# Kernel tuning notes

Measured on AMD Instinct MI355X. Metric: run time of the kernel, lower is better.

## Reference

```python
import jax, jax.numpy as jnp
import numpy as np

N_NODES = 100000


def _gcn_norm(edge_index, n):
    # PyG GCNConv default: add self-loops, symmetric normalization
    src, dst = edge_index[0], edge_index[1]
    loops = jnp.arange(n, dtype=src.dtype)
    src = jnp.concatenate([src, loops])
    dst = jnp.concatenate([dst, loops])
    deg = jax.ops.segment_sum(jnp.ones_like(dst, dtype=jnp.float32), dst, num_segments=n)
    dinv = jnp.where(deg > 0, jax.lax.rsqrt(deg), 0.0)
    norm = dinv[src] * dinv[dst]  # [E+N]
    return src, dst, norm


def _gcn_conv(x, src, dst, norm, W, b, n):
    h = x @ W                                  # [N, out] transform first
    msg = h[src] * norm[:, None]               # gather + edge weight
    out = jax.ops.segment_sum(msg, dst, num_segments=n)  # scatter-add
    return out + b


def setup_inputs() -> dict:
    key = jax.random.key(0)
    k1, k2, k3, k4 = jax.random.split(key, 4)
    in_f, h_f, out_f = 128, 256, 128
    x = jax.random.normal(k1, (N_NODES, in_f), dtype=jnp.float32)
    edge_index = jax.random.randint(k2, (2, 1600000), 0, N_NODES, dtype=jnp.int64)
    W1 = jax.random.normal(k3, (in_f, h_f), dtype=jnp.float32) / np.sqrt(in_f)
    b1 = jnp.zeros((h_f,), dtype=jnp.float32)
    W2 = jax.random.normal(k4, (h_f, out_f), dtype=jnp.float32) / np.sqrt(h_f)
    b2 = jnp.zeros((out_f,), dtype=jnp.float32)
    return {"x": x, "edge_index": edge_index, "W1": W1, "b1": b1, "W2": W2, "b2": b2}


def reference(x, edge_index, W1, b1, W2, b2):
    n = x.shape[0]
    src, dst, norm = _gcn_norm(edge_index, n)
    h = jax.nn.relu(_gcn_conv(x, src, dst, norm, W1, b1, n))
    return _gcn_conv(h, src, dst, norm, W2, b2, n)
```

## Files before the change

kernel.cpp:

```cpp
#include <hip/hip_runtime.h>

typedef __bf16 bf16x8 __attribute__((ext_vector_type(8)));
typedef float f32x4 __attribute__((ext_vector_type(4)));

#define DEVI static __device__ __forceinline__
#define SCH 8192
#define CAP 49152

DEVI unsigned short f2bf(float f){
  unsigned int x = __builtin_bit_cast(unsigned int, f);
  x = (x + 0x7fffu + ((x >> 16) & 1u)) >> 16;
  return (unsigned short)x;
}
DEVI unsigned int packbf2(float a, float b){
  return (unsigned int)f2bf(a) | ((unsigned int)f2bf(b) << 16);
}
DEVI float bflo(unsigned int u){ return __builtin_bit_cast(float, u << 16); }
DEVI float bfhi(unsigned int u){ return __builtin_bit_cast(float, u & 0xffff0000u); }

__global__ void k_zero(int* __restrict__ p, int n){
  int i = blockIdx.x*256 + threadIdx.x;
  if (i < n) p[i] = 0;
}


__global__ __launch_bounds__(512) void kb_scat1h(const int* __restrict__ src,
    const int* __restrict__ dst, int* __restrict__ cntf, int* __restrict__ cntc,
    int* __restrict__ p1, int E, int NB, int NBC){
  __shared__ int hf[2048];
  __shared__ int baseSh[64];
  __shared__ int hc[64];
  int t = threadIdx.x;
  for (int i=t;i<NB;i+=512) hf[i]=0;
  __syncthreads();
  int base = blockIdx.x*SCH;
  int lim = base+SCH < E ? base+SCH : E;
  for (int i = base+t; i < lim; i += 512)
    atomicAdd(&hf[dst[i]>>8], 1);
  __syncthreads();
  if (t < NBC){
    int s2 = 0;
    int f0 = t*8;
    for (int j=0;j<8;j++){ int f=f0+j; if (f<NB) s2 += hf[f]; }
    baseSh[t] = s2 ? atomicAdd(&cntc[t], s2) : 0;
    hc[t] = 0;
  }
  for (int i=t;i<NB;i+=512)
    if (hf[i]) atomicAdd(&cntf[i], hf[i]);
  __syncthreads();
  for (int i = base+t; i < lim; i += 512){
    int d = dst[i];
    int b = d>>11;
    int r = atomicAdd(&hc[b], 1);
    p1[(size_t)b*CAP + baseSh[b] + r] = (src[i]<<11) | (d & 2047);
  }
}

__global__ __launch_bounds__(256) void kb_scan(const int* __restrict__ cntf,
    int* __restrict__ bucketOff, int* __restrict__ bucketCur, int NB){
  __shared__ int sh[256];
  int t = threadIdx.x;
  int per = (NB+255)/256;
  int vals[8];
  int lsum = 0;
  for (int j=0;j<per;j++){
    int i = t*per+j;
    int v = (i<NB) ? cntf[i] : 0;
    vals[j]=v; lsum+=v;
  }
  sh[t]=lsum; __syncthreads();
  for (int off=1; off<256; off<<=1){
    int x = (t>=off) ? sh[t-off] : 0;
    __syncthreads();
    sh[t] += x;
    __syncthreads();
  }
  int run = sh[t]-lsum;
  for (int j=0;j<per;j++){
    int i = t*per+j;
    if (i<NB){ bucketOff[i]=run; bucketCur[i]=run; }
    run += vals[j];
  }
  if (t==255) bucketOff[NB]=run;
}

__global__ __launch_bounds__(512) void kb_scat2(const int* __restrict__ p1,
    const int* __restrict__ cntc, int* __restrict__ cur,
    int* __restrict__ pk, int NB){
  __shared__ int h[8];
  __shared__ int baseSh[8];
  int t = threadIdx.x;
  int bc = blockIdx.x >> 3;
  int sub = blockIdx.x & 7;
  int s = bc*CAP;
  int e = s + cntc[bc];
  if (t < 8) h[t] = 0;
  __syncthreads();
  for (int i = s + sub*512 + t; i < e; i += 4096)
    atomicAdd(&h[(p1[i]>>8)&7], 1);
  __syncthreads();
  if (t < 8){
    int c2 = h[t];
    baseSh[t] = c2 ? atomicAdd(&cur[bc*8+t], c2) : 0;
    h[t] = 0;
  }
  __syncthreads();
  for (int i = s + sub*512 + t; i < e; i += 4096){
    int p = p1[i];
    int f = (p>>8)&7;
    int r = atomicAdd(&h[f], 1);
    int pos = baseSh[f] + r;
    pk[pos] = ((p>>11)<<8) | (p&255);
  }
}

DEVI void packW(const float* __restrict__ W, unsigned short* __restrict__ Wp,
                int idx, int N, int NF){
  int l = idx & 63;
  int frag = idx >> 6;
  int cf = frag % NF;
  int ks = frag / NF;
  int kbase = ks*32 + (l>>4)*8;
  int col = cf*16 + (l&15);
  unsigned short* dp = Wp + (size_t)idx*8;
  #pragma unroll
  for (int j=0;j<8;j++) dp[j] = f2bf(W[(size_t)(kbase+j)*N + col]);
}

__global__ __launch_bounds__(256) void kb_fused(const int* __restrict__ pk,
    const int* __restrict__ bOff,
    int* __restrict__ rp, int* __restrict__ csr, float* __restrict__ dinv,
    const float2* __restrict__ x2, unsigned int* __restrict__ xb,
    const float* __restrict__ W1, unsigned short* __restrict__ W1p,
    const float* __restrict__ W2, unsigned short* __restrict__ W2p,
    int n, int NB, int E){
  int t = threadIdx.x;
  int b = blockIdx.x;
  if (b >= NB){
    int idx = (b-NB)*256 + t;
    if (idx < 4096) packW(W1, W1p, idx, 256, 16);
    else            packW(W2, W2p, idx-4096, 128, 8);
    return;
  }
  __shared__ int c[256];
  __shared__ int sh[256];
  __shared__ int cur[256];
  __shared__ float dv[256];
  int s = bOff[b], e2 = bOff[b+1];
  c[t]=0; __syncthreads();
  for (int i=s+t;i<e2;i+=256) atomicAdd(&c[pk[i]&255], 1);
  __syncthreads();
  int deg = c[t];
  sh[t]=deg; __syncthreads();
  for (int o=1;o<256;o<<=1){
    int x = (t>=o) ? sh[t-o] : 0;
    __syncthreads();
    sh[t]+=x;
    __syncthreads();
  }
  int excl = sh[t]-deg;
  int node = b*256+t;
  float dnv = rsqrtf((float)(deg+1));
  if (node<n){
    rp[node] = s + excl;
    dinv[node] = dnv;
  }
  if (b==NB-1 && t==0) rp[n] = E;
  cur[t] = s + excl;
  dv[t] = dnv;
  __syncthreads();
  for (int i=s+t;i<e2;i+=256){
    int p = pk[i];
    int r = atomicAdd(&cur[p&255], 1);
    csr[r] = p & (int)0xFFFFFF00u;
  }
  int base_node = b*256;
  int rows = n - base_node; if (rows > 256) rows = 256;
  int j = t & 63;
  for (int rb = t>>6; rb < rows; rb += 4){
    int nd = base_node + rb;
    float d = dv[rb];
    float2 v = x2[(size_t)nd*64 + j];
    xb[(size_t)nd*64 + j] = packbf2(d*v.x, d*v.y);
  }
}

#define ACC8(V) { a0+=bflo(V.x); a1+=bfhi(V.x); a2+=bflo(V.y); a3+=bfhi(V.y); \
                  a4+=bflo(V.z); a5+=bfhi(V.z); a6+=bflo(V.w); a7+=bfhi(V.w); }

template<bool FINAL>
__global__ __launch_bounds__(256) void k_agg(
    const unsigned int* __restrict__ xs, const int* __restrict__ rp,
    const int* __restrict__ csr, const float* __restrict__ dinv,
    const float* __restrict__ bias, unsigned int* __restrict__ outb,
    float* __restrict__ outf, int n){
  int node = blockIdx.x*4 + (threadIdx.x>>6);
  if (node >= n) return;
  int l = threadIdx.x & 63;
  int q = l & 15;
  int h = l >> 4;
  const char* xbase = (const char*)xs;
  float a0=0,a1=0,a2=0,a3=0,a4=0,a5=0,a6=0,a7=0;
  int e = rp[node], end = rp[node+1];
  int p = e;
  int nf = (end - e) >> 4;
  for (int blk=0; blk<nf; ++blk, p+=16){
    uint4 v[4];
    #pragma unroll
    for (int i=0;i<4;i++){
      int boff = csr[p + 4*i + h];
      v[i] = *(const uint4*)(xbase + (size_t)(unsigned)boff + q*16);
    }
    ACC8(v[0]); ACC8(v[1]); ACC8(v[2]); ACC8(v[3]);
  }
  int rem = end - p;
  if (rem >= 8){
    uint4 v[2];
    #pragma unroll
    for (int i=0;i<2;i++){
      int boff = csr[p + 4*i + h];
      v[i] = *(const uint4*)(xbase + (size_t)(unsigned)boff + q*16);
    }
    ACC8(v[0]); ACC8(v[1]);
    p += 8; rem -= 8;
  }
  if (rem > 0){
    uint4 v[2];
    #pragma unroll
    for (int i=0;i<2;i++){
      int ei = p + 4*i + h;
      int ec = ei < end-1 ? ei : end-1;
      int boff = csr[ec];
      uint4 t = *(const uint4*)(xbase + (size_t)(unsigned)boff + q*16);
      if (ei >= end){ t.x=0; t.y=0; t.z=0; t.w=0; }
      v[i] = t;
    }
    ACC8(v[0]); ACC8(v[1]);
  }
  a0 += __shfl_xor(a0,16); a0 += __shfl_xor(a0,32);
  a1 += __shfl_xor(a1,16); a1 += __shfl_xor(a1,32);
  a2 += __shfl_xor(a2,16); a2 += __shfl_xor(a2,32);
  a3 += __shfl_xor(a3,16); a3 += __shfl_xor(a3,32);
  a4 += __shfl_xor(a4,16); a4 += __shfl_xor(a4,32);
  a5 += __shfl_xor(a5,16); a5 += __shfl_xor(a5,32);
  a6 += __shfl_xor(a6,16); a6 += __shfl_xor(a6,32);
  a7 += __shfl_xor(a7,16); a7 += __shfl_xor(a7,32);
  uint4 sv = *(const uint4*)(xbase + (size_t)node*256 + q*16);
  ACC8(sv);
  float dn = dinv[node];
  if constexpr (FINAL){
    if (h < 2){
      const float4 bb = *(const float4*)(bias + 8*q + 4*h);
      f32x4 r;
      r.x = (h ? a4 : a0)*dn + bb.x;
      r.y = (h ? a5 : a1)*dn + bb.y;
      r.z = (h ? a6 : a2)*dn + bb.z;
      r.w = (h ? a7 : a3)*dn + bb.w;
      __builtin_nontemporal_store(r, (f32x4*)(outf + (size_t)node*128 + 8*q + 4*h));
    }
  } else {
    if (h == 0){
      uint4 o;
      o.x = packbf2(a0*dn, a1*dn);
      o.y = packbf2(a2*dn, a3*dn);
      o.z = packbf2(a4*dn, a5*dn);
      o.w = packbf2(a6*dn, a7*dn);
      *(uint4*)((char*)outb + (size_t)node*256 + q*16) = o;
    }
  }
}

DEVI int ldsaddr(int row, int colg ){
  int gs = (colg & ~7) | ((colg & 7) ^ (row & 7));
  return row*512 + gs*16;
}

__global__ __launch_bounds__(256) void k_mlp(
    const unsigned short* __restrict__ A, const unsigned short* __restrict__ W1p,
    const float* __restrict__ b1, const unsigned short* __restrict__ W2p,
    const float* __restrict__ dinv, unsigned short* __restrict__ T, int M){
  __shared__ unsigned char At[64*512];
  int l = threadIdx.x & 63;
  int w = threadIdx.x >> 6;
  int r0 = blockIdx.x*64;
  int lr = l & 15, lg = l >> 4;
  int c0 = w*64;
  {
    f32x4 acc[4][4];
    #pragma unroll
    for (int i=0;i<4;i++)
      #pragma unroll
      for (int j=0;j<4;j++)
        acc[i][j] = f32x4{0.f,0.f,0.f,0.f};
    #pragma unroll
    for (int ks=0; ks<4; ++ks){
      bf16x8 a[4], b[4];
      #pragma unroll
      for (int ar=0;ar<4;ar++){
        int row = r0 + ar*16 + lr;
        if (row > M-1) row = M-1;
        const uint4* p = (const uint4*)(A + (size_t)row*128 + ks*32 + lg*8);
        union { uint4 u; bf16x8 v; } t; t.u = *p; a[ar] = t.v;
      }
      #pragma unroll
      for (int cb=0;cb<4;cb++){
        int cf = (c0>>4) + cb;
        const uint4* p = (const uint4*)(W1p + ((size_t)(ks*16 + cf)*64 + l)*8);
        union { uint4 u; bf16x8 v; } t; t.u = *p; b[cb] = t.v;
      }
      #pragma unroll
      for (int ar=0;ar<4;ar++)
        #pragma unroll
        for (int cb=0;cb<4;cb++)
          acc[ar][cb] = __builtin_amdgcn_mfma_f32_16x16x32_bf16(a[ar], b[cb], acc[ar][cb], 0, 0, 0);
    }
    #pragma unroll
    for (int ar=0;ar<4;ar++){
      #pragma unroll
      for (int i=0;i<4;i++){
        int row = ar*16 + lg*4 + i;
        #pragma unroll
        for (int cb=0;cb<4;cb++){
          int col = c0 + cb*16 + lr;
          float v = acc[ar][cb][i] + b1[col];
          v = fmaxf(v, 0.f);
          *(unsigned short*)(At + ldsaddr(row, col>>3) + (col&7)*2) = f2bf(v);
        }
      }
    }
  }
  __syncthreads();
  {
    f32x4 acc[4][2];
    #pragma unroll
    for (int i=0;i<4;i++){
      acc[i][0] = f32x4{0.f,0.f,0.f,0.f};
      acc[i][1] = f32x4{0.f,0.f,0.f,0.f};
    }
    #pragma unroll
    for (int ks=0; ks<8; ++ks){
      bf16x8 a[4], b[2];
      #pragma unroll
      for (int ar=0;ar<4;ar++){
        int row = ar*16 + lr;
        union { uint4 u; bf16x8 v; } t;
        t.u = *(const uint4*)(At + ldsaddr(row, ks*4 + lg));
        a[ar] = t.v;
      }
      #pragma unroll
      for (int cb=0;cb<2;cb++){
        int cf = w*2 + cb;
        const uint4* p = (const uint4*)(W2p + ((size_t)(ks*8 + cf)*64 + l)*8);
        union { uint4 u; bf16x8 v; } t; t.u = *p; b[cb] = t.v;
      }
      #pragma unroll
      for (int ar=0;ar<4;ar++){
        acc[ar][0] = __builtin_amdgcn_mfma_f32_16x16x32_bf16(a[ar], b[0], acc[ar][0], 0, 0, 0);
        acc[ar][1] = __builtin_amdgcn_mfma_f32_16x16x32_bf16(a[ar], b[1], acc[ar][1], 0, 0, 0);
      }
    }
    #pragma unroll
    for (int ar=0;ar<4;ar++){
      #pragma unroll
      for (int i=0;i<4;i++){
        int row = r0 + ar*16 + lg*4 + i;
        if (row < M){
          float rs = dinv[row];
          #pragma unroll
          for (int cb=0;cb<2;cb++){
            int col = w*32 + cb*16 + lr;
            T[(size_t)row*128 + col] = f2bf(acc[ar][cb][i] * rs);
          }
        }
      }
    }
  }
}

extern "C" void kernel_launch(void* const* d_in, const int* in_sizes, int n_in,
                              void* d_out, int out_size, void* d_ws, size_t ws_size,
                              hipStream_t stream){
  const float* x  = (const float*)d_in[0];
  const int*   ei = (const int*)d_in[1];
  const float* W1 = (const float*)d_in[2];
  const float* b1 = (const float*)d_in[3];
  const float* W2 = (const float*)d_in[4];
  const float* b2 = (const float*)d_in[5];
  const int IN_F = 128;
  int n = in_sizes[0] / IN_F;
  int E = in_sizes[1] / 2;
  const int* srcI = ei;
  const int* dstI = ei + E;
  const int NB  = (n+255)>>8;
  const int NBC = (n+2047)>>11;

  char* ws = (char*)d_ws;
  size_t off = 0;
  auto alloc = [&](size_t bytes)->char*{
    char* p = ws + off; off += (bytes + 255) & ~(size_t)255; return p;
  };
  int*   rp    = (int*)  alloc(((size_t)n+1)*4);
  float* dinv  = (float*)alloc((size_t)n*4);
  int*   cntf  = (int*)  alloc(((size_t)NB+NBC)*4);
  int*   cntc  = cntf + NB;
  int*   bOff  = (int*)  alloc(((size_t)NB+1)*4);
  int*   bCur  = (int*)  alloc((size_t)NB*4);
  unsigned short* W1p = (unsigned short*)alloc((size_t)128*256*2);
  unsigned short* W2p = (unsigned short*)alloc((size_t)256*128*2);
  int*   csr   = (int*)  alloc((size_t)E*4);
  unsigned int* xb = (unsigned int*)alloc((size_t)n*64*4);
  unsigned int* AX = (unsigned int*)alloc((size_t)n*64*4);
  int*   p1    = (int*)  alloc((size_t)NBC*CAP*4);
  int*   pk    = (int*)  alloc((size_t)E*4);

  int NSC = (E + SCH - 1)/SCH;

  k_zero<<<(NB+NBC+255)/256,256,0,stream>>>(cntf, NB+NBC);
  kb_scat1h<<<NSC,512,0,stream>>>(srcI, dstI, cntf, cntc, p1, E, NB, NBC);
  kb_scan<<<1,256,0,stream>>>(cntf, bOff, bCur, NB);
  kb_scat2<<<NBC*8,512,0,stream>>>(p1, cntc, bCur, pk, NB);
  kb_fused<<<NB+32,256,0,stream>>>(pk, bOff, rp, csr, dinv,
                                   (const float2*)x, xb, W1, W1p, W2, W2p, n, NB, E);
  k_agg<false><<<(n+3)/4,256,0,stream>>>(xb, rp, csr, dinv, nullptr, AX, nullptr, n);
  unsigned int* T = xb;
  k_mlp<<<(n+63)/64,256,0,stream>>>((const unsigned short*)AX, W1p, b1, W2p,
                                    dinv, (unsigned short*)T, n);
  k_agg<true><<<(n+3)/4,256,0,stream>>>(T, rp, csr, dinv, b2, nullptr, (float*)d_out, n);
}
```

Baseline: 232.2 us.

## Slice feature matrices into 8 column slabs for cache-local aggregation

Stores the bf16 feature matrices as 8 column slices of 16 features (32 bytes per node per slice) instead of row-major 256-byte rows. The aggregation kernel now gives each block one slice, with 8 lanes per node each gathering 4 bytes per neighbour, so the gathered working set per slice (about 3.2 MB) can stay in L2. The MLP kernel's loads and stores are changed to read and write the sliced layout. In exchange, each gather is a small 32-byte access and the CSR indices are read 8 times, once per slice. The 16-edge vector unrolling and the cross-lane reductions are also removed.

```diff
diff --git a/kernel.cpp b/kernel.cpp
--- a/kernel.cpp
+++ b/kernel.cpp
@@ -172,101 +172,58 @@
   for (int i=s+t;i<e2;i+=256){
     int p = pk[i];
     int r = atomicAdd(&cur[p&255], 1);
-    csr[r] = p & (int)0xFFFFFF00u;
+    csr[r] = (p >> 8) << 5;
   }
   int base_node = b*256;
   int rows = n - base_node; if (rows > 256) rows = 256;
   int j = t & 63;
+  int sl = j >> 3;
+  int off = j & 7;
   for (int rb = t>>6; rb < rows; rb += 4){
     int nd = base_node + rb;
     float d = dv[rb];
     float2 v = x2[(size_t)nd*64 + j];
-    xb[(size_t)nd*64 + j] = packbf2(d*v.x, d*v.y);
-  }
-}
-
-#define ACC8(V) { a0+=bflo(V.x); a1+=bfhi(V.x); a2+=bflo(V.y); a3+=bfhi(V.y); \
-                  a4+=bflo(V.z); a5+=bfhi(V.z); a6+=bflo(V.w); a7+=bfhi(V.w); }
+    xb[(((size_t)sl)*n + nd)*8 + off] = packbf2(d*v.x, d*v.y);
+  }
+}
 
 template<bool FINAL>
-__global__ __launch_bounds__(256) void k_agg(
+__global__ __launch_bounds__(256) void k_aggs(
     const unsigned int* __restrict__ xs, const int* __restrict__ rp,
     const int* __restrict__ csr, const float* __restrict__ dinv,
     const float* __restrict__ bias, unsigned int* __restrict__ outb,
     float* __restrict__ outf, int n){
-  int node = blockIdx.x*4 + (threadIdx.x>>6);
+  int bid = blockIdx.x;
+  int sl = bid & 7;
+  int w = threadIdx.x >> 6;
+  int l = threadIdx.x & 63;
+  int g = l >> 3;
+  int k = l & 7;
+  int node = (bid >> 3)*32 + w*8 + g;
   if (node >= n) return;
-  int l = threadIdx.x & 63;
-  int q = l & 15;
-  int h = l >> 4;
-  const char* xbase = (const char*)xs;
-  float a0=0,a1=0,a2=0,a3=0,a4=0,a5=0,a6=0,a7=0;
+  const char* sbase = (const char*)xs + (size_t)sl * n * 32;
+  float a0 = 0.f, a1 = 0.f;
   int e = rp[node], end = rp[node+1];
-  int p = e;
-  int nf = (end - e) >> 4;
-  for (int blk=0; blk<nf; ++blk, p+=16){
-    uint4 v[4];
-    #pragma unroll
-    for (int i=0;i<4;i++){
-      int boff = csr[p + 4*i + h];
-      v[i] = *(const uint4*)(xbase + (size_t)(unsigned)boff + q*16);
-    }
-    ACC8(v[0]); ACC8(v[1]); ACC8(v[2]); ACC8(v[3]);
-  }
-  int rem = end - p;
-  if (rem >= 8){
-    uint4 v[2];
-    #pragma unroll
-    for (int i=0;i<2;i++){
-      int boff = csr[p + 4*i + h];
-      v[i] = *(const uint4*)(xbase + (size_t)(unsigned)boff + q*16);
-    }
-    ACC8(v[0]); ACC8(v[1]);
-    p += 8; rem -= 8;
-  }
-  if (rem > 0){
-    uint4 v[2];
-    #pragma unroll
-    for (int i=0;i<2;i++){
-      int ei = p + 4*i + h;
+  for (int p = e; p < end; p += 4){
+    #pragma unroll
+    for (int u = 0; u < 4; ++u){
+      int ei = p + u;
       int ec = ei < end-1 ? ei : end-1;
       int boff = csr[ec];
-      uint4 t = *(const uint4*)(xbase + (size_t)(unsigned)boff + q*16);
-      if (ei >= end){ t.x=0; t.y=0; t.z=0; t.w=0; }
-      v[i] = t;
-    }
-    ACC8(v[0]); ACC8(v[1]);
-  }
-  a0 += __shfl_xor(a0,16); a0 += __shfl_xor(a0,32);
-  a1 += __shfl_xor(a1,16); a1 += __shfl_xor(a1,32);
-  a2 += __shfl_xor(a2,16); a2 += __shfl_xor(a2,32);
-  a3 += __shfl_xor(a3,16); a3 += __shfl_xor(a3,32);
-  a4 += __shfl_xor(a4,16); a4 += __shfl_xor(a4,32);
-  a5 += __shfl_xor(a5,16); a5 += __shfl_xor(a5,32);
-  a6 += __shfl_xor(a6,16); a6 += __shfl_xor(a6,32);
-  a7 += __shfl_xor(a7,16); a7 += __shfl_xor(a7,32);
-  uint4 sv = *(const uint4*)(xbase + (size_t)node*256 + q*16);
-  ACC8(sv);
+      unsigned int v = *(const unsigned int*)(sbase + (size_t)(unsigned)boff + k*4);
+      if (ei >= end) v = 0;
+      a0 += bflo(v); a1 += bfhi(v);
+    }
+  }
+  unsigned int sv = *(const unsigned int*)(sbase + (size_t)node*32 + k*4);
+  a0 += bflo(sv); a1 += bfhi(sv);
   float dn = dinv[node];
   if constexpr (FINAL){
-    if (h < 2){
-      const float4 bb = *(const float4*)(bias + 8*q + 4*h);
-      f32x4 r;
-      r.x = (h ? a4 : a0)*dn + bb.x;
-      r.y = (h ? a5 : a1)*dn + bb.y;
-      r.z = (h ? a6 : a2)*dn + bb.z;
-      r.w = (h ? a7 : a3)*dn + bb.w;
-      __builtin_nontemporal_store(r, (f32x4*)(outf + (size_t)node*128 + 8*q + 4*h));
-    }
+    float2 bb = *(const float2*)(bias + sl*16 + k*2);
+    float2 r; r.x = a0*dn + bb.x; r.y = a1*dn + bb.y;
+    *(float2*)(outf + (size_t)node*128 + sl*16 + k*2) = r;
   } else {
-    if (h == 0){
-      uint4 o;
-      o.x = packbf2(a0*dn, a1*dn);
-      o.y = packbf2(a2*dn, a3*dn);
-      o.z = packbf2(a4*dn, a5*dn);
-      o.w = packbf2(a6*dn, a7*dn);
-      *(uint4*)((char*)outb + (size_t)node*256 + q*16) = o;
-    }
+    outb[((size_t)sl*n + node)*8 + k] = packbf2(a0*dn, a1*dn);
   }
 }
 
@@ -299,7 +256,8 @@
       for (int ar=0;ar<4;ar++){
         int row = r0 + ar*16 + lr;
         if (row > M-1) row = M-1;
-        const uint4* p = (const uint4*)(A + (size_t)row*128 + ks*32 + lg*8);
+        int s2 = 2*ks + (lg>>1);
+        const uint4* p = (const uint4*)((const char*)A + ((size_t)s2*M + row)*32 + (lg&1)*16);
         union { uint4 u; bf16x8 v; } t; t.u = *p; a[ar] = t.v;
       }
       #pragma unroll
@@ -369,7 +327,7 @@
           #pragma unroll
           for (int cb=0;cb<2;cb++){
             int col = w*32 + cb*16 + lr;
-            T[(size_t)row*128 + col] = f2bf(acc[ar][cb][i] * rs);
+            T[((size_t)(col>>4)*M + row)*16 + (col&15)] = f2bf(acc[ar][cb][i] * rs);
           }
         }
       }
@@ -421,9 +379,10 @@
   kb_scat2<<<NBC*8,512,0,stream>>>(p1, cntc, bCur, pk, NB);
   kb_fused<<<NB+32,256,0,stream>>>(pk, bOff, rp, csr, dinv,
                                    (const float2*)x, xb, W1, W1p, W2, W2p, n, NB, E);
-  k_agg<false><<<(n+3)/4,256,0,stream>>>(xb, rp, csr, dinv, nullptr, AX, nullptr, n);
+  int gagg = ((n+31)/32)*8;
+  k_aggs<false><<<gagg,256,0,stream>>>(xb, rp, csr, dinv, nullptr, AX, nullptr, n);
   unsigned int* T = xb;
   k_mlp<<<(n+63)/64,256,0,stream>>>((const unsigned short*)AX, W1p, b1, W2p,
                                     dinv, (unsigned short*)T, n);
-  k_agg<true><<<(n+3)/4,256,0,stream>>>(T, rp, csr, dinv, b2, nullptr, (float*)d_out, n);
-}
+  k_aggs<true><<<gagg,256,0,stream>>>(T, rp, csr, dinv, b2, nullptr, (float*)d_out, n);
+}
```

Measured after the change: 337.8 us. +45.5%, slower.
